# Performance work log

Measured on AMD Instinct MI355X. Metric: run time of the kernel, lower is better.

Reference implementation:

```python
import jax, jax.numpy as jnp
import numpy as np

VOCAB, H, MAXLEN = 50257, 1024, 128


def setup_inputs() -> dict:
    key = jax.random.key(0)
    ks = jax.random.split(key, 14)
    s = 0.02  # init scale
    f32 = jnp.float32
    return {
        "x": jax.random.randint(ks[0], (1,), 0, VOCAB),
        "h": jax.random.normal(ks[1], (1, 1, H), f32),
        "encoder_outputs": jax.random.normal(ks[2], (MAXLEN, H), f32),
        "emb": jax.random.normal(ks[3], (VOCAB, H), f32) * s,
        "W_attn": jax.random.normal(ks[4], (MAXLEN, 2 * H), f32) * s,
        "b_attn": jnp.zeros((MAXLEN,), f32),
        "W_comb": jax.random.normal(ks[5], (H, 2 * H), f32) * s,
        "b_comb": jnp.zeros((H,), f32),
        "w_ih": jax.random.normal(ks[6], (3 * H, H), f32) * s,
        "w_hh": jax.random.normal(ks[7], (3 * H, H), f32) * s,
        "b_ih": jnp.zeros((3 * H,), f32),
        "b_hh": jnp.zeros((3 * H,), f32),
        "W_out": jax.random.normal(ks[8], (VOCAB, H), f32) * s,
        "b_out": jnp.zeros((VOCAB,), f32),
    }


def reference(x, h, encoder_outputs, emb, W_attn, b_attn, W_comb, b_comb,
              w_ih, w_hh, b_ih, b_hh, W_out, b_out):
    # Single decode step (batch=1, seq=1); dropout in eval mode (identity).
    e = emb[x]                       # [1, H] embedded token
    h0 = h[0]                        # [1, H] hidden state
    # attention over encoder outputs
    attn_w = jax.nn.softmax(jnp.concatenate([e, h0], axis=1) @ W_attn.T + b_attn, axis=1)  # [1, MAXLEN]
    attn_applied = attn_w @ encoder_outputs                                                 # [1, H]
    # combine + relu
    g = jax.nn.relu(jnp.concatenate([e, attn_applied], axis=1) @ W_comb.T + b_comb)        # [1, H]
    # single-step GRU (PyTorch gate order: r, z, n)
    gi = g @ w_ih.T + b_ih           # [1, 3H]
    gh = h0 @ w_hh.T + b_hh          # [1, 3H]
    i_r, i_z, i_n = jnp.split(gi, 3, axis=1)
    h_r, h_z, h_n = jnp.split(gh, 3, axis=1)
    r = jax.nn.sigmoid(i_r + h_r)
    z = jax.nn.sigmoid(i_z + h_z)
    n = jnp.tanh(i_n + r * h_n)
    h_new = (1.0 - z) * n + z * h0   # [1, H]
    out = jax.nn.log_softmax(h_new @ W_out.T + b_out, axis=1)  # [1, VOCAB]
    return out, h_new[None], attn_w
```

## Files before the change

kernel.cpp:

```cpp
#include <hip/hip_runtime.h>
#include <math.h>

#define H 1024
#define MAXLEN 128
#define VOCAB 50257

#define ROWS_PB 8
#define NB_OUT ((VOCAB + ROWS_PB - 1) / ROWS_PB)

__device__ inline float wave_reduce_sum(float v) {
    #pragma unroll
    for (int off = 32; off > 0; off >>= 1) v += __shfl_down(v, off);
    return v;
}

__device__ inline float dot4(float4 a, float4 b) {
    return a.x * b.x + a.y * b.y + a.z * b.z + a.w * b.w;
}

__global__ void k_attn_logits(const int* x, const float* h, const float* emb,
                              const float* W_attn, const float* b_attn, float* logits) {
    const int lane = threadIdx.x & 63, wid = threadIdx.x >> 6;
    const int row = blockIdx.x * 4 + wid;
    const float4* w4 = (const float4*)(W_attn + row * (2 * H));
    const float4* e4 = (const float4*)(emb + (long long)x[0] * H);
    const float4* h4 = (const float4*)h;
    float acc = 0.f;
    #pragma unroll
    for (int i = 0; i < 8; i++) {
        int idx = lane + i * 64;
        float4 wv = w4[idx];
        float4 cv = (idx < 256) ? e4[idx] : h4[idx - 256];
        acc += dot4(wv, cv);
    }
    acc = wave_reduce_sum(acc);
    if (lane == 0) logits[row] = acc + b_attn[row];
}

__global__ void k_attn_sm_apply(const float* logits, const float* enc,
                                float* attn_applied, float* out_attn) {
    __shared__ float buf[MAXLEN];
    __shared__ float wsm[MAXLEN];
    int t = threadIdx.x;
    if (t < MAXLEN) buf[t] = logits[t];
    __syncthreads();
    float m = -INFINITY;
    #pragma unroll 8
    for (int k = 0; k < MAXLEN; k++) m = fmaxf(m, buf[k]);
    if (t < MAXLEN) wsm[t] = expf(buf[t] - m);
    __syncthreads();
    float s = 0.f;
    #pragma unroll 8
    for (int k = 0; k < MAXLEN; k++) s += wsm[k];
    float inv = 1.f / s;
    if (t < MAXLEN) {
        int j = blockIdx.x * MAXLEN + t;
        float acc = 0.f;
        #pragma unroll 8
        for (int k = 0; k < MAXLEN; k++) acc += wsm[k] * enc[k * H + j];
        attn_applied[j] = acc * inv;
        if (blockIdx.x == 0) out_attn[t] = wsm[t] * inv;
    }
}

__global__ void k_combine(const int* x, const float* emb, const float* attn_applied,
                          const float* W_comb, const float* b_comb, float* g) {
    int wid = threadIdx.x >> 6, lane = threadIdx.x & 63;
    int row = blockIdx.x * 4 + wid;
    const float4* w4 = (const float4*)(W_comb + (long long)row * (2 * H));
    const float4* e4 = (const float4*)(emb + (long long)x[0] * H);
    const float4* a4 = (const float4*)attn_applied;
    float acc = 0.f;
    #pragma unroll
    for (int i = 0; i < 8; i++) {
        int idx = lane + i * 64;
        float4 wv = w4[idx];
        float4 cv = (idx < 256) ? e4[idx] : a4[idx - 256];
        acc += dot4(wv, cv);
    }
    acc = wave_reduce_sum(acc);
    if (lane == 0) g[row] = fmaxf(acc + b_comb[row], 0.f);
}

__global__ void k_gru_fused(const float* g, const float* h,
                            const float* w_ih, const float* w_hh,
                            const float* b_ih, const float* b_hh, float* h_new) {
    const int j = blockIdx.x, t = threadIdx.x;
    const int lane = t & 63, wid = t >> 6;
    __shared__ float red6[4][6];
    const float4* g4 = (const float4*)g;
    const float4* h4 = (const float4*)h;
    float4 vg = g4[t];
    float4 vh = h4[t];
    float a6[6];
    #pragma unroll
    for (int gt = 0; gt < 3; gt++) {
        const float4* wi = (const float4*)(w_ih + (long long)(j + gt * H) * H);
        const float4* wh = (const float4*)(w_hh + (long long)(j + gt * H) * H);
        a6[gt]     = dot4(wi[t], vg);
        a6[3 + gt] = dot4(wh[t], vh);
    }
    #pragma unroll
    for (int k = 0; k < 6; k++) {
        float v = a6[k];
        #pragma unroll
        for (int off = 32; off > 0; off >>= 1) v += __shfl_down(v, off);
        if (lane == 0) red6[wid][k] = v;
    }
    __syncthreads();
    if (t == 0) {
        float d[6];
        #pragma unroll
        for (int k = 0; k < 6; k++)
            d[k] = red6[0][k] + red6[1][k] + red6[2][k] + red6[3][k];
        float gi_r = d[0] + b_ih[j];
        float gi_z = d[1] + b_ih[j + H];
        float gi_n = d[2] + b_ih[j + 2 * H];
        float gh_r = d[3] + b_hh[j];
        float gh_z = d[4] + b_hh[j + H];
        float gh_n = d[5] + b_hh[j + 2 * H];
        float r = 1.f / (1.f + expf(-(gi_r + gh_r)));
        float z = 1.f / (1.f + expf(-(gi_z + gh_z)));
        float n = tanhf(gi_n + r * gh_n);
        h_new[j] = (1.f - z) * n + z * h[j];
    }
}

__global__ void k_out_matvec(const float* hn, const float* W_out, const float* b_out,
                             float* out, float* pmax, float* psum) {
    const int t = threadIdx.x;
    const int lane = t & 63, wid = t >> 6;
    const int row0 = blockIdx.x * ROWS_PB + wid * 2;
    __shared__ float lm[ROWS_PB];

    const float4* h4 = (const float4*)hn;
    float4 hreg[4];
    #pragma unroll
    for (int i = 0; i < 4; i++) hreg[i] = h4[lane + i * 64];

    float l0 = -INFINITY, l1 = -INFINITY;
    if (row0 + 1 < VOCAB) {
        const float4* w0 = (const float4*)(W_out + (long long)row0 * H);
        const float4* w1 = (const float4*)(W_out + (long long)(row0 + 1) * H);
        float4 a0[4], a1[4];
        #pragma unroll
        for (int i = 0; i < 4; i++) a0[i] = w0[lane + i * 64];
        #pragma unroll
        for (int i = 0; i < 4; i++) a1[i] = w1[lane + i * 64];
        float acc0 = 0.f, acc1 = 0.f;
        #pragma unroll
        for (int i = 0; i < 4; i++) { acc0 += dot4(a0[i], hreg[i]); acc1 += dot4(a1[i], hreg[i]); }
        acc0 = wave_reduce_sum(acc0);
        acc1 = wave_reduce_sum(acc1);
        if (lane == 0) {
            l0 = acc0 + b_out[row0];
            l1 = acc1 + b_out[row0 + 1];
            out[row0] = l0;
            out[row0 + 1] = l1;
        }
    } else {
        for (int r = row0; r < VOCAB && r < row0 + 2; r++) {
            const float4* w4 = (const float4*)(W_out + (long long)r * H);
            float acc = 0.f;
            #pragma unroll
            for (int i = 0; i < 4; i++) acc += dot4(w4[lane + i * 64], hreg[i]);
            acc = wave_reduce_sum(acc);
            if (lane == 0) {
                float lv = acc + b_out[r];
                out[r] = lv;
                if (r == row0) l0 = lv; else l1 = lv;
            }
        }
    }
    if (lane == 0) { lm[wid * 2] = l0; lm[wid * 2 + 1] = l1; }
    __syncthreads();
    if (t == 0) {
        float m = -INFINITY;
        #pragma unroll
        for (int i = 0; i < ROWS_PB; i++) m = fmaxf(m, lm[i]);
        float s = 0.f;
        #pragma unroll
        for (int i = 0; i < ROWS_PB; i++)
            if (lm[i] != -INFINITY) s += expf(lm[i] - m);
        pmax[blockIdx.x] = m;
        psum[blockIdx.x] = s;
    }
}

__global__ void k_lse_merge(const float* pmax, const float* psum, float* c) {
    __shared__ float red[16];
    __shared__ float Msh;
    int lane = threadIdx.x & 63, wid = threadIdx.x >> 6;
    float m = -INFINITY;
    for (int i = threadIdx.x; i < NB_OUT; i += blockDim.x) m = fmaxf(m, pmax[i]);
    #pragma unroll
    for (int off = 32; off > 0; off >>= 1) m = fmaxf(m, __shfl_down(m, off));
    if (lane == 0) red[wid] = m;
    __syncthreads();
    if (threadIdx.x == 0) {
        float mm = red[0];
        for (int i = 1; i < 16; i++) mm = fmaxf(mm, red[i]);
        Msh = mm;
    }
    __syncthreads();
    float M = Msh;
    float s = 0.f;
    for (int i = threadIdx.x; i < NB_OUT; i += blockDim.x) s += psum[i] * expf(pmax[i] - M);
    s = wave_reduce_sum(s);
    if (lane == 0) red[wid] = s;
    __syncthreads();
    if (threadIdx.x == 0) {
        float ss = 0.f;
        for (int i = 0; i < 16; i++) ss += red[i];
        c[0] = M + logf(ss);
    }
}

__global__ void k_sub(float* out, const float* c) {
    int v = blockIdx.x * blockDim.x + threadIdx.x;
    if (v < VOCAB) out[v] -= c[0];
}

extern "C" void kernel_launch(void* const* d_in, const int* in_sizes, int n_in,
                              void* d_out, int out_size, void* d_ws, size_t ws_size,
                              hipStream_t stream) {
    const int*   x     = (const int*)d_in[0];
    const float* h     = (const float*)d_in[1];
    const float* enc   = (const float*)d_in[2];
    const float* emb   = (const float*)d_in[3];
    const float* W_attn= (const float*)d_in[4];
    const float* b_attn= (const float*)d_in[5];
    const float* W_comb= (const float*)d_in[6];
    const float* b_comb= (const float*)d_in[7];
    const float* w_ih  = (const float*)d_in[8];
    const float* w_hh  = (const float*)d_in[9];
    const float* b_ih  = (const float*)d_in[10];
    const float* b_hh  = (const float*)d_in[11];
    const float* W_out = (const float*)d_in[12];
    const float* b_out = (const float*)d_in[13];

    float* out      = (float*)d_out;
    float* out_h    = out + VOCAB;
    float* out_attn = out + VOCAB + H;

    float* ws          = (float*)d_ws;
    float* logits128   = ws;
    float* attn_applied= ws + 256;
    float* g_vec       = ws + 1280;
    float* lse_c       = ws + 2304;
    float* pmax        = ws + 4096;
    float* psum        = ws + 12288;

    k_attn_logits<<<MAXLEN / 4, 256, 0, stream>>>(x, h, emb, W_attn, b_attn, logits128);
    k_attn_sm_apply<<<H / MAXLEN, 256, 0, stream>>>(logits128, enc, attn_applied, out_attn);
    k_combine<<<H / 4, 256, 0, stream>>>(x, emb, attn_applied, W_comb, b_comb, g_vec);
    k_gru_fused<<<H, 256, 0, stream>>>(g_vec, h, w_ih, w_hh, b_ih, b_hh, out_h);
    k_out_matvec<<<NB_OUT, 256, 0, stream>>>(out_h, W_out, b_out, out, pmax, psum);
    k_lse_merge<<<1, 1024, 0, stream>>>(pmax, psum, lse_c);
    k_sub<<<(VOCAB + 1023) / 1024, 1024, 0, stream>>>(out, lse_c);
}
```

Before: 71.31 us.

## Restructure decode pipeline: hoist w_hh matvec, fuse softmax-apply with combine, merge LSE+sub

The h-dependent GRU matvec (w_hh·h) moves into the first kernel alongside the attention logits, since it does not depend on the attention result. Softmax-apply and the combine matvec are fused into one kernel: each of 64 blocks recomputes the full attention-applied vector into shared memory, then does 16 W_comb rows. The GRU kernel then only does the w_ih matvec, one wave per output. The LSE merge and subtraction are fused, with every block redundantly recomputing the global log-sum-exp. Together these cut the launch count from seven to five and take the w_hh work off the serial chain, at the cost of redundant enc reads and duplicated reductions.

```diff
diff --git a/kernel.cpp b/kernel.cpp
--- a/kernel.cpp
+++ b/kernel.cpp
@@ -7,6 +7,10 @@
 
 #define ROWS_PB 8
 #define NB_OUT ((VOCAB + ROWS_PB - 1) / ROWS_PB)
+#define NB_GH 768
+#define NB_K1 (NB_GH + 32)
+#define NB_K2 64
+#define NB_SUB ((VOCAB + 1023) / 1024)
 
 __device__ inline float wave_reduce_sum(float v) {
     #pragma unroll
@@ -18,30 +22,49 @@
     return a.x * b.x + a.y * b.y + a.z * b.z + a.w * b.w;
 }
 
-__global__ void k_attn_logits(const int* x, const float* h, const float* emb,
-                              const float* W_attn, const float* b_attn, float* logits) {
+__global__ void k_pre(const int* x, const float* h, const float* emb,
+                      const float* W_attn, const float* b_attn,
+                      const float* w_hh, const float* b_hh,
+                      float* gh, float* logits) {
     const int lane = threadIdx.x & 63, wid = threadIdx.x >> 6;
-    const int row = blockIdx.x * 4 + wid;
-    const float4* w4 = (const float4*)(W_attn + row * (2 * H));
-    const float4* e4 = (const float4*)(emb + (long long)x[0] * H);
     const float4* h4 = (const float4*)h;
-    float acc = 0.f;
-    #pragma unroll
-    for (int i = 0; i < 8; i++) {
-        int idx = lane + i * 64;
-        float4 wv = w4[idx];
-        float4 cv = (idx < 256) ? e4[idx] : h4[idx - 256];
-        acc += dot4(wv, cv);
-    }
-    acc = wave_reduce_sum(acc);
-    if (lane == 0) logits[row] = acc + b_attn[row];
-}
-
-__global__ void k_attn_sm_apply(const float* logits, const float* enc,
-                                float* attn_applied, float* out_attn) {
+    if (blockIdx.x < NB_GH) {
+        int row = blockIdx.x * 4 + wid;
+        const float4* w4 = (const float4*)(w_hh + (long long)row * H);
+        float acc = 0.f;
+        #pragma unroll
+        for (int i = 0; i < 4; i++) {
+            int idx = lane + i * 64;
+            acc += dot4(w4[idx], h4[idx]);
+        }
+        acc = wave_reduce_sum(acc);
+        if (lane == 0) gh[row] = acc + b_hh[row];
+    } else {
+        int row = (blockIdx.x - NB_GH) * 4 + wid;
+        const float4* w4 = (const float4*)(W_attn + row * (2 * H));
+        const float4* e4 = (const float4*)(emb + (long long)x[0] * H);
+        float acc = 0.f;
+        #pragma unroll
+        for (int i = 0; i < 8; i++) {
+            int idx = lane + i * 64;
+            float4 wv = w4[idx];
+            float4 cv = (idx < 256) ? e4[idx] : h4[idx - 256];
+            acc += dot4(wv, cv);
+        }
+        acc = wave_reduce_sum(acc);
+        if (lane == 0) logits[row] = acc + b_attn[row];
+    }
+}
+
+__global__ void k_sm_combine(const int* x, const float* emb, const float* logits,
+                             const float* enc, const float* W_comb, const float* b_comb,
+                             float* g_vec, float* out_attn) {
     __shared__ float buf[MAXLEN];
     __shared__ float wsm[MAXLEN];
-    int t = threadIdx.x;
+    __shared__ float attn[H] __attribute__((aligned(16)));
+    const int t = threadIdx.x;
+    const int lane = t & 63, wid = t >> 6;
+
     if (t < MAXLEN) buf[t] = logits[t];
     __syncthreads();
     float m = -INFINITY;
@@ -52,73 +75,66 @@
     float s = 0.f;
     #pragma unroll 8
     for (int k = 0; k < MAXLEN; k++) s += wsm[k];
-    float inv = 1.f / s;
-    if (t < MAXLEN) {
-        int j = blockIdx.x * MAXLEN + t;
+    const float inv = 1.f / s;
+
+    #pragma unroll
+    for (int jj = 0; jj < 4; jj++) {
+        int j = jj * 256 + t;
         float acc = 0.f;
         #pragma unroll 8
         for (int k = 0; k < MAXLEN; k++) acc += wsm[k] * enc[k * H + j];
-        attn_applied[j] = acc * inv;
-        if (blockIdx.x == 0) out_attn[t] = wsm[t] * inv;
-    }
-}
-
-__global__ void k_combine(const int* x, const float* emb, const float* attn_applied,
-                          const float* W_comb, const float* b_comb, float* g) {
-    int wid = threadIdx.x >> 6, lane = threadIdx.x & 63;
-    int row = blockIdx.x * 4 + wid;
-    const float4* w4 = (const float4*)(W_comb + (long long)row * (2 * H));
+        attn[j] = acc * inv;
+    }
+    if (blockIdx.x == 0 && t < MAXLEN) out_attn[t] = wsm[t] * inv;
+    __syncthreads();
+
     const float4* e4 = (const float4*)(emb + (long long)x[0] * H);
-    const float4* a4 = (const float4*)attn_applied;
-    float acc = 0.f;
-    #pragma unroll
-    for (int i = 0; i < 8; i++) {
-        int idx = lane + i * 64;
-        float4 wv = w4[idx];
-        float4 cv = (idx < 256) ? e4[idx] : a4[idx - 256];
-        acc += dot4(wv, cv);
-    }
-    acc = wave_reduce_sum(acc);
-    if (lane == 0) g[row] = fmaxf(acc + b_comb[row], 0.f);
-}
-
-__global__ void k_gru_fused(const float* g, const float* h,
-                            const float* w_ih, const float* w_hh,
-                            const float* b_ih, const float* b_hh, float* h_new) {
-    const int j = blockIdx.x, t = threadIdx.x;
-    const int lane = t & 63, wid = t >> 6;
-    __shared__ float red6[4][6];
-    const float4* g4 = (const float4*)g;
-    const float4* h4 = (const float4*)h;
-    float4 vg = g4[t];
-    float4 vh = h4[t];
-    float a6[6];
+    const float4* a4 = (const float4*)attn;
+    #pragma unroll
+    for (int r = 0; r < 4; r++) {
+        int row = blockIdx.x * 16 + wid * 4 + r;
+        const float4* w4 = (const float4*)(W_comb + (long long)row * (2 * H));
+        float acc = 0.f;
+        #pragma unroll
+        for (int i = 0; i < 8; i++) {
+            int idx = lane + i * 64;
+            float4 wv = w4[idx];
+            float4 cv = (idx < 256) ? e4[idx] : a4[idx - 256];
+            acc += dot4(wv, cv);
+        }
+        acc = wave_reduce_sum(acc);
+        if (lane == 0) g_vec[row] = fmaxf(acc + b_comb[row], 0.f);
+    }
+}
+
+__global__ void k_gru(const float* g_vec, const float* h, const float* gh,
+                      const float* w_ih, const float* b_ih, const float* b_hh_unused,
+                      float* h_new) {
+    const int lane = threadIdx.x & 63, wid = threadIdx.x >> 6;
+    const int j = blockIdx.x * 4 + wid;
+    const float4* g4 = (const float4*)g_vec;
+    float4 vg[4];
+    #pragma unroll
+    for (int i = 0; i < 4; i++) vg[i] = g4[lane + i * 64];
+
+    float a3[3];
     #pragma unroll
     for (int gt = 0; gt < 3; gt++) {
         const float4* wi = (const float4*)(w_ih + (long long)(j + gt * H) * H);
-        const float4* wh = (const float4*)(w_hh + (long long)(j + gt * H) * H);
-        a6[gt]     = dot4(wi[t], vg);
-        a6[3 + gt] = dot4(wh[t], vh);
-    }
-    #pragma unroll
-    for (int k = 0; k < 6; k++) {
-        float v = a6[k];
-        #pragma unroll
-        for (int off = 32; off > 0; off >>= 1) v += __shfl_down(v, off);
-        if (lane == 0) red6[wid][k] = v;
-    }
-    __syncthreads();
-    if (t == 0) {
-        float d[6];
-        #pragma unroll
-        for (int k = 0; k < 6; k++)
-            d[k] = red6[0][k] + red6[1][k] + red6[2][k] + red6[3][k];
-        float gi_r = d[0] + b_ih[j];
-        float gi_z = d[1] + b_ih[j + H];
-        float gi_n = d[2] + b_ih[j + 2 * H];
-        float gh_r = d[3] + b_hh[j];
-        float gh_z = d[4] + b_hh[j + H];
-        float gh_n = d[5] + b_hh[j + 2 * H];
+        float acc = 0.f;
+        #pragma unroll
+        for (int i = 0; i < 4; i++) acc += dot4(wi[lane + i * 64], vg[i]);
+        a3[gt] = acc;
+    }
+    #pragma unroll
+    for (int k = 0; k < 3; k++) a3[k] = wave_reduce_sum(a3[k]);
+    if (lane == 0) {
+        float gi_r = a3[0] + b_ih[j];
+        float gi_z = a3[1] + b_ih[j + H];
+        float gi_n = a3[2] + b_ih[j + 2 * H];
+        float gh_r = gh[j];
+        float gh_z = gh[j + H];
+        float gh_n = gh[j + 2 * H];
         float r = 1.f / (1.f + expf(-(gi_r + gh_r)));
         float z = 1.f / (1.f + expf(-(gi_z + gh_z)));
         float n = tanhf(gi_n + r * gh_n);
@@ -187,38 +203,41 @@
     }
 }
 
-__global__ void k_lse_merge(const float* pmax, const float* psum, float* c) {
+__global__ void k_merge_sub(const float* pmax, const float* psum, float* out) {
     __shared__ float red[16];
     __shared__ float Msh;
-    int lane = threadIdx.x & 63, wid = threadIdx.x >> 6;
+    const int t = threadIdx.x;
+    const int lane = t & 63, wid = t >> 6;
     float m = -INFINITY;
-    for (int i = threadIdx.x; i < NB_OUT; i += blockDim.x) m = fmaxf(m, pmax[i]);
+    for (int i = t; i < NB_OUT; i += 1024) m = fmaxf(m, pmax[i]);
     #pragma unroll
     for (int off = 32; off > 0; off >>= 1) m = fmaxf(m, __shfl_down(m, off));
     if (lane == 0) red[wid] = m;
     __syncthreads();
-    if (threadIdx.x == 0) {
+    if (t == 0) {
         float mm = red[0];
+        #pragma unroll
         for (int i = 1; i < 16; i++) mm = fmaxf(mm, red[i]);
         Msh = mm;
     }
     __syncthreads();
-    float M = Msh;
+    const float M = Msh;
     float s = 0.f;
-    for (int i = threadIdx.x; i < NB_OUT; i += blockDim.x) s += psum[i] * expf(pmax[i] - M);
+    for (int i = t; i < NB_OUT; i += 1024) s += psum[i] * expf(pmax[i] - M);
     s = wave_reduce_sum(s);
+    __syncthreads();
     if (lane == 0) red[wid] = s;
     __syncthreads();
-    if (threadIdx.x == 0) {
+    if (t == 0) {
         float ss = 0.f;
+        #pragma unroll
         for (int i = 0; i < 16; i++) ss += red[i];
-        c[0] = M + logf(ss);
-    }
-}
-
-__global__ void k_sub(float* out, const float* c) {
-    int v = blockIdx.x * blockDim.x + threadIdx.x;
-    if (v < VOCAB) out[v] -= c[0];
+        Msh = M + logf(ss);
+    }
+    __syncthreads();
+    const float c = Msh;
+    int v = blockIdx.x * 1024 + t;
+    if (v < VOCAB) out[v] -= c;
 }
 
 extern "C" void kernel_launch(void* const* d_in, const int* in_sizes, int n_in,
@@ -245,17 +264,16 @@
 
     float* ws          = (float*)d_ws;
     float* logits128   = ws;
-    float* attn_applied= ws + 256;
-    float* g_vec       = ws + 1280;
-    float* lse_c       = ws + 2304;
-    float* pmax        = ws + 4096;
-    float* psum        = ws + 12288;
-
-    k_attn_logits<<<MAXLEN / 4, 256, 0, stream>>>(x, h, emb, W_attn, b_attn, logits128);
-    k_attn_sm_apply<<<H / MAXLEN, 256, 0, stream>>>(logits128, enc, attn_applied, out_attn);
-    k_combine<<<H / 4, 256, 0, stream>>>(x, emb, attn_applied, W_comb, b_comb, g_vec);
-    k_gru_fused<<<H, 256, 0, stream>>>(g_vec, h, w_ih, w_hh, b_ih, b_hh, out_h);
+    float* g_vec       = ws + 256;
+    float* gh          = ws + 1536;
+    float* pmax        = ws + 8192;
+    float* psum        = ws + 16384;
+
+    k_pre<<<NB_K1, 256, 0, stream>>>(x, h, emb, W_attn, b_attn, w_hh, b_hh,
+                                     gh, logits128);
+    k_sm_combine<<<NB_K2, 256, 0, stream>>>(x, emb, logits128, enc,
+                                            W_comb, b_comb, g_vec, out_attn);
+    k_gru<<<H / 4, 256, 0, stream>>>(g_vec, h, gh, w_ih, b_ih, b_hh, out_h);
     k_out_matvec<<<NB_OUT, 256, 0, stream>>>(out_h, W_out, b_out, out, pmax, psum);
-    k_lse_merge<<<1, 1024, 0, stream>>>(pmax, psum, lse_c);
-    k_sub<<<(VOCAB + 1023) / 1024, 1024, 0, stream>>>(out, lse_c);
-}
+    k_merge_sub<<<NB_SUB, 1024, 0, stream>>>(pmax, psum, out);
+}
```

After: 85.90 us. 1.2x slower.
